# Optimization experiments

Hardware: AMD Instinct MI355X
Metric: run time of the kernel (lower is better)

## Reference

```python
import jax, jax.numpy as jnp
import numpy as np

N, F, B = 16384, 512, 4
H = 4          # attn heads
MR = 2         # mlp_ratio
GH = max(F // 4, 32)   # gate hidden = 128
SE = F // 8    # SE bottleneck
FH = 512       # fusion_hidden
E = 3          # num experts
EPS = 1e-5


def setup_inputs() -> dict:
    key = jax.random.key(0)
    ks = jax.random.split(key, 24)
    p = lambda k, s: 0.02 * jax.random.normal(k, s, dtype=jnp.float32)
    return {
        'branches': jax.random.normal(ks[0], (N, F, B), dtype=jnp.float32),
        'conv_pw_w': p(ks[1], (F, F)),          # Conv1d k=1, no bias
        'conv_dw_w': p(ks[2], (F, 3)),          # depthwise k=3
        'gn_w': jnp.ones((F,), jnp.float32), 'gn_b': jnp.zeros((F,), jnp.float32),
        'se_w1': p(ks[3], (SE, F)), 'se_w2': p(ks[4], (F, SE)),
        'ln_attn_w': jnp.ones((F,), jnp.float32), 'ln_attn_b': jnp.zeros((F,), jnp.float32),
        'in_proj_w': p(ks[5], (3 * F, F)), 'in_proj_b': jnp.zeros((3 * F,), jnp.float32),
        'attn_out_w': p(ks[6], (F, F)), 'attn_out_b': jnp.zeros((F,), jnp.float32),
        'ln_ffn_w': jnp.ones((F,), jnp.float32), 'ln_ffn_b': jnp.zeros((F,), jnp.float32),
        'ffn_w1': p(ks[7], (MR * F, F)), 'ffn_b1': jnp.zeros((MR * F,), jnp.float32),
        'ffn_w2': p(ks[8], (F, MR * F)), 'ffn_b2': jnp.zeros((F,), jnp.float32),
        'mlp_ln_w': jnp.ones((F,), jnp.float32), 'mlp_ln_b': jnp.zeros((F,), jnp.float32),
        'mlp_w1': p(ks[9], (MR * F, F)), 'mlp_b1': jnp.zeros((MR * F,), jnp.float32),
        'mlp_w2': p(ks[10], (F, MR * F)), 'mlp_b2': jnp.zeros((F,), jnp.float32),
        'gate_w1': p(ks[11], (GH, 2 * F)), 'gate_b1': jnp.zeros((GH,), jnp.float32),
        'gate_w2': p(ks[12], (E, GH)), 'gate_b2': jnp.zeros((E,), jnp.float32),
        'outp_w': p(ks[13], (FH, F)),
    }


def _ln(x, w, b):
    m = jnp.mean(x, -1, keepdims=True)
    v = jnp.mean((x - m) ** 2, -1, keepdims=True)
    return (x - m) * jax.lax.rsqrt(v + EPS) * w + b


def _gelu(x):
    return jax.nn.gelu(x, approximate=False)


def _forward(branches, conv_pw_w, conv_dw_w, gn_w, gn_b, se_w1, se_w2,
             ln_attn_w, ln_attn_b, in_proj_w, in_proj_b, attn_out_w, attn_out_b,
             ln_ffn_w, ln_ffn_b, ffn_w1, ffn_b1, ffn_w2, ffn_b2,
             mlp_ln_w, mlp_ln_b, mlp_w1, mlp_b1, mlp_w2, mlp_b2,
             gate_w1, gate_b1, gate_w2, gate_b2, outp_w):
    # ---- Conv expert ----
    x1 = jnp.einsum('fg,ngb->nfb', conv_pw_w, branches)          # pointwise conv
    xp = jnp.pad(x1, ((0, 0), (0, 0), (1, 1)))                    # depthwise k=3, pad=1
    w0, w1, w2 = (conv_dw_w[:, k][None, :, None] for k in range(3))
    x1 = w0 * xp[:, :, :-2] + w1 * xp[:, :, 1:-1] + w2 * xp[:, :, 2:]
    s = jnp.mean(x1, -1)                                          # SE squeeze (N,F)
    s = jax.nn.sigmoid(jax.nn.relu(s @ se_w1.T) @ se_w2.T)
    x1 = x1 * s[:, :, None]
    m = jnp.mean(x1, (1, 2), keepdims=True)                       # GroupNorm(1 group)
    v = jnp.mean((x1 - m) ** 2, (1, 2), keepdims=True)
    x1 = (x1 - m) * jax.lax.rsqrt(v + EPS) * gn_w[None, :, None] + gn_b[None, :, None]
    x1 = _gelu(x1)
    # ---- Attention expert (branches as tokens) ----
    t = jnp.swapaxes(branches, 1, 2)                              # (N,B,F)
    h = _ln(t, ln_attn_w, ln_attn_b)
    qkv = h @ in_proj_w.T + in_proj_b
    q, k, vv = jnp.split(qkv, 3, axis=-1)
    dh = F // H
    q = q.reshape(N, B, H, dh) * (dh ** -0.5)
    k = k.reshape(N, B, H, dh)
    vv = vv.reshape(N, B, H, dh)
    att = jax.nn.softmax(jnp.einsum('nqhd,nkhd->nhqk', q, k), axis=-1)
    ao = jnp.einsum('nhqk,nkhd->nqhd', att, vv).reshape(N, B, F)
    t = t + ao @ attn_out_w.T + attn_out_b
    h = _ln(t, ln_ffn_w, ln_ffn_b)
    t = t + _gelu(h @ ffn_w1.T + ffn_b1) @ ffn_w2.T + ffn_b2
    x2 = jnp.swapaxes(t, 1, 2)
    # ---- MLP expert ----
    t3 = jnp.swapaxes(branches, 1, 2)
    h3 = _ln(t3, mlp_ln_w, mlp_ln_b)
    t3 = t3 + _gelu(h3 @ mlp_w1.T + mlp_b1) @ mlp_w2.T + mlp_b2
    x3 = jnp.swapaxes(t3, 1, 2)
    # ---- Gating ----
    ctx = jnp.concatenate([jnp.mean(branches, -1), jnp.max(branches, -1)], axis=-1)
    logits = _gelu(ctx @ gate_w1.T + gate_b1) @ gate_w2.T + gate_b2
    alpha = jax.nn.softmax(logits, axis=-1)                       # (N,3)
    fused = (alpha[:, 0, None, None] * x1 + alpha[:, 1, None, None] * x2
             + alpha[:, 2, None, None] * x3)
    return jnp.einsum('of,nfb->nob', outp_w, fused)               # out_proj k=1 conv


def reference(branches, conv_pw_w, conv_dw_w, gn_w, gn_b, se_w1, se_w2,
              ln_attn_w, ln_attn_b, in_proj_w, in_proj_b, attn_out_w, attn_out_b,
              ln_ffn_w, ln_ffn_b, ffn_w1, ffn_b1, ffn_w2, ffn_b2,
              mlp_ln_w, mlp_ln_b, mlp_w1, mlp_b1, mlp_w2, mlp_b2,
              gate_w1, gate_b1, gate_w2, gate_b2, outp_w):
    return _forward(branches, conv_pw_w, conv_dw_w, gn_w, gn_b, se_w1, se_w2,
                    ln_attn_w, ln_attn_b, in_proj_w, in_proj_b, attn_out_w, attn_out_b,
                    ln_ffn_w, ln_ffn_b, ffn_w1, ffn_b1, ffn_w2, ffn_b2,
                    mlp_ln_w, mlp_ln_b, mlp_w1, mlp_b1, mlp_w2, mlp_b2,
                    gate_w1, gate_b1, gate_w2, gate_b2, outp_w)
```

## Files before the change

kernel.cpp:

```cpp
#include <hip/hip_runtime.h>
#include <math.h>


#define N_TOT 16384
#define EPSV 1e-5f

typedef unsigned short u16;
typedef unsigned int   u32;
typedef __attribute__((ext_vector_type(8))) short  short8;
typedef __attribute__((ext_vector_type(4))) float  floatx4;

__device__ __forceinline__ float gelu_exact(float x) {
    return 0.5f * x * (1.0f + erff(x * 0.70710678118654752440f));
}
__device__ __forceinline__ float wave_sum(float v) {
    #pragma unroll
    for (int o = 32; o > 0; o >>= 1) v += __shfl_xor(v, o);
    return v;
}
__device__ __forceinline__ u16 f2bf(float f) {
    u32 u = __float_as_uint(f);
    return (u16)((u + 0x7fffu + ((u >> 16) & 1u)) >> 16);
}
__device__ __forceinline__ u32 pack2(float lo, float hi) {
    return (u32)f2bf(lo) | ((u32)f2bf(hi) << 16);
}
__device__ __forceinline__ float bf1f(u16 u) { return __uint_as_float((u32)u << 16); }
__device__ __forceinline__ float2 bf2f2(u32 u) {
    return make_float2(__uint_as_float(u << 16), __uint_as_float(u & 0xffff0000u));
}
__device__ __forceinline__ void gload_lds16(const void* g, void* l) {
    __builtin_amdgcn_global_load_lds(
        (const __attribute__((address_space(1))) unsigned int*)g,
        (__attribute__((address_space(3))) unsigned int*)l, 16, 0, 0);
}

#define BARR() asm volatile("s_barrier" ::: "memory")
#define VMW(N) asm volatile("s_waitcnt vmcnt(" #N ")" ::: "memory")

#define W_CONVPW 0
#define W_INPROJ 262144
#define W_ATTNO  1048576
#define W_FFN1   1310720
#define W_FFN2   1835008
#define W_MLP1   2359296
#define W_MLP2   2883584
#define W_GATE1  3407872
#define W_SE1    3538944
#define W_SE2    3571712
#define W_OUTP   3604480
#define W_TOT    3866624

__global__ __launch_bounds__(256) void k_w2b(
        const float* __restrict__ p0, const float* __restrict__ p1,
        const float* __restrict__ p2, const float* __restrict__ p3,
        const float* __restrict__ p4, const float* __restrict__ p5,
        const float* __restrict__ p6, const float* __restrict__ p7,
        const float* __restrict__ p8, const float* __restrict__ p9,
        const float* __restrict__ p10, u16* __restrict__ dst)
{
    int i = blockIdx.x * 256 + threadIdx.x;
    if (i >= W_TOT) return;
    const float* s; int off;
    if      (i < W_INPROJ) { s = p0;  off = W_CONVPW; }
    else if (i < W_ATTNO)  { s = p1;  off = W_INPROJ; }
    else if (i < W_FFN1)   { s = p2;  off = W_ATTNO; }
    else if (i < W_FFN2)   { s = p3;  off = W_FFN1; }
    else if (i < W_MLP1)   { s = p4;  off = W_FFN2; }
    else if (i < W_MLP2)   { s = p5;  off = W_MLP1; }
    else if (i < W_GATE1)  { s = p6;  off = W_MLP2; }
    else if (i < W_SE1)    { s = p7;  off = W_GATE1; }
    else if (i < W_SE2)    { s = p8;  off = W_SE1; }
    else if (i < W_OUTP)   { s = p9;  off = W_SE2; }
    else                   { s = p10; off = W_OUTP; }
    dst[i] = f2bf(s[i - off]);
}

__global__ __launch_bounds__(256) void k_prep_ln(const float* __restrict__ br,
        int baseN, u16* __restrict__ Tb, u16* __restrict__ CTX,
        const float* __restrict__ law, const float* __restrict__ lab, u16* __restrict__ LNA,
        const float* __restrict__ lmw, const float* __restrict__ lmb, u16* __restrict__ LNM)
{
    __shared__ float lds[4][516];
    int t = threadIdx.x;
    const float* p = br + (size_t)(baseN + blockIdx.x) * 2048;
    u16* c = CTX + (size_t)blockIdx.x * 1024;
    #pragma unroll
    for (int i = 0; i < 2; ++i) {
        int f = t + i * 256;
        float4 v = *(const float4*)(p + f * 4);
        lds[0][f] = v.x; lds[1][f] = v.y; lds[2][f] = v.z; lds[3][f] = v.w;
        c[f]       = f2bf((v.x + v.y + v.z + v.w) * 0.25f);
        c[512 + f] = f2bf(fmaxf(fmaxf(v.x, v.y), fmaxf(v.z, v.w)));
    }
    __syncthreads();
    int b = t >> 6, lane = t & 63, f0 = lane * 8;
    float xv[8];
    #pragma unroll
    for (int i = 0; i < 8; ++i) xv[i] = lds[b][f0 + i];
    float s = 0.f;
    #pragma unroll
    for (int i = 0; i < 8; ++i) s += xv[i];
    s = wave_sum(s);
    float m = s * (1.f / 512.f);
    float q = 0.f;
    #pragma unroll
    for (int i = 0; i < 8; ++i) { float d = xv[i] - m; q += d * d; }
    q = wave_sum(q);
    float rs = rsqrtf(q * (1.f / 512.f) + EPSV);
    size_t row = (size_t)blockIdx.x * 4 + b;
    *(uint4*)(Tb + row * 512 + f0) = make_uint4(pack2(xv[0], xv[1]), pack2(xv[2], xv[3]),
                                                pack2(xv[4], xv[5]), pack2(xv[6], xv[7]));
    float o[8];
    #pragma unroll
    for (int i = 0; i < 8; ++i) o[i] = (xv[i] - m) * rs * law[f0 + i] + lab[f0 + i];
    *(uint4*)(LNA + row * 512 + f0) = make_uint4(pack2(o[0], o[1]), pack2(o[2], o[3]),
                                                 pack2(o[4], o[5]), pack2(o[6], o[7]));
    #pragma unroll
    for (int i = 0; i < 8; ++i) o[i] = (xv[i] - m) * rs * lmw[f0 + i] + lmb[f0 + i];
    *(uint4*)(LNM + row * 512 + f0) = make_uint4(pack2(o[0], o[1]), pack2(o[2], o[3]),
                                                 pack2(o[4], o[5]), pack2(o[6], o[7]));
}

__global__ __launch_bounds__(256) void k_ln_b(const u16* __restrict__ X,
        const float* __restrict__ w, const float* __restrict__ b, u16* __restrict__ O)
{
    int t = threadIdx.x;
    int wave = t >> 6, lane = t & 63;
    size_t r = (size_t)blockIdx.x * 4 + wave;
    int f0 = lane * 8;
    uint4 raw = *(const uint4*)(X + r * 512 + f0);
    float xv[8];
    { float2 a = bf2f2(raw.x); xv[0] = a.x; xv[1] = a.y; }
    { float2 a = bf2f2(raw.y); xv[2] = a.x; xv[3] = a.y; }
    { float2 a = bf2f2(raw.z); xv[4] = a.x; xv[5] = a.y; }
    { float2 a = bf2f2(raw.w); xv[6] = a.x; xv[7] = a.y; }
    float s = 0.f;
    #pragma unroll
    for (int i = 0; i < 8; ++i) s += xv[i];
    s = wave_sum(s);
    float m = s * (1.f / 512.f);
    float q = 0.f;
    #pragma unroll
    for (int i = 0; i < 8; ++i) { float d = xv[i] - m; q += d * d; }
    q = wave_sum(q);
    float rs = rsqrtf(q * (1.f / 512.f) + EPSV);
    float o[8];
    #pragma unroll
    for (int i = 0; i < 8; ++i) o[i] = (xv[i] - m) * rs * w[f0 + i] + b[f0 + i];
    *(uint4*)(O + r * 512 + f0) = make_uint4(pack2(o[0], o[1]), pack2(o[2], o[3]),
                                             pack2(o[4], o[5]), pack2(o[6], o[7]));
}


#define STAGE(SLOT, TILE) do {                                                \
    const u16* sm_ = ((SLOT) < 2) ? A : W;                                    \
    int rb_ = (((SLOT) < 2) ? m0 : n0) + ((SLOT) & 1) * 128;                  \
    int k0_ = (TILE) * 64;                                                    \
    u16* db_ = lds + (((TILE) & 1) * 32768) + (SLOT) * 8192;                  \
    _Pragma("unroll")                                                         \
    for (int l_ = 0; l_ < 2; ++l_) {                                          \
        int L_ = (l_ * 512 + tid) * 16;                                       \
        int row_ = L_ >> 7;                                                   \
        int ir_ = (L_ & 127) ^ ((row_ & 7) << 4);                             \
        gload_lds16(sm_ + (size_t)(rb_ + row_) * K + k0_ + (ir_ >> 1),        \
                    db_ + (L_ >> 1));                                         \
    } } while (0)

#define QUAD(MH, NH, STAGESTMT) do {                                          \
    const u16* lb_ = lds + cur * 32768;                                       \
    short8 a_[4][2], b_[2][2];                                                \
    _Pragma("unroll")                                                         \
    for (int mi = 0; mi < 4; ++mi)                                            \
        _Pragma("unroll")                                                     \
        for (int ks = 0; ks < 2; ++ks)                                        \
            a_[mi][ks] = *(const short8*)(lb_ + (MH) * 8192 + arow[mi] + gcol[ks]); \
    _Pragma("unroll")                                                         \
    for (int ni = 0; ni < 2; ++ni)                                            \
        _Pragma("unroll")                                                     \
        for (int ks = 0; ks < 2; ++ks)                                        \
            b_[ni][ks] = *(const short8*)(lb_ + 16384 + (NH) * 8192 + brow[ni] + gcol[ks]); \
    STAGESTMT;                                                                \
    BARR();                                                                   \
    __builtin_amdgcn_s_setprio(1);                                            \
    _Pragma("unroll")                                                         \
    for (int ks = 0; ks < 2; ++ks)                                            \
        _Pragma("unroll")                                                     \
        for (int mi = 0; mi < 4; ++mi)                                        \
            _Pragma("unroll")                                                 \
            for (int ni = 0; ni < 2; ++ni)                                    \
                acc[MH][NH][mi][ni] = __builtin_amdgcn_mfma_f32_16x16x32_bf16( \
                    a_[mi][ks], b_[ni][ks], acc[MH][NH][mi][ni], 0, 0, 0);    \
    __builtin_amdgcn_s_setprio(0);                                            \
} while (0)

template<int EPI, bool HAS_BIAS, bool HAS_RES, int STORE>
__global__ __launch_bounds__(512, 2) void k_gemm256(
        const u16* __restrict__ A, const u16* __restrict__ W,
        const float* __restrict__ bias, const u16* __restrict__ Res,
        void* __restrict__ Cout, int Ncols, int K, int baseN, int nTX)
{
    __shared__ __align__(16) u16 lds[65536];
    const int tid = threadIdx.x;
    const int wid = tid >> 6, lane = tid & 63;
    const int lr = lane & 15, kg = lane >> 4;
    const int wm = (wid >> 2) * 64;
    const int wn = (wid & 3) * 32;

    int nwg = gridDim.x, orig = blockIdx.x;
    int q = nwg >> 3, r = nwg & 7;
    int xcd = orig & 7, lin = orig >> 3;
    int wgid = (xcd < r ? xcd * (q + 1) : r * (q + 1) + (xcd - r) * q) + lin;
    const int m0 = (wgid / nTX) * 256, n0 = (wgid % nTX) * 256;

    int arow[4], brow[2], gcol[2];
    #pragma unroll
    for (int mi = 0; mi < 4; ++mi) arow[mi] = (wm + mi * 16 + lr) * 64;
    #pragma unroll
    for (int ni = 0; ni < 2; ++ni) brow[ni] = (wn + ni * 16 + lr) * 64;
    #pragma unroll
    for (int ks = 0; ks < 2; ++ks) gcol[ks] = (ks * 32 + kg * 8) ^ ((lr & 7) << 3);

    floatx4 acc[2][2][4][2] = {};

    STAGE(0, 0); STAGE(2, 0); STAGE(1, 0); STAGE(3, 0);

    const int NT = K >> 6;
    int cur = 0;
    for (int t = 0; t < NT - 1; ++t) {
        int nx = t + 1;
        VMW(4); BARR(); QUAD(0, 0, STAGE(0, nx));
        VMW(4); BARR(); QUAD(1, 0, STAGE(2, nx));
        VMW(4); BARR(); QUAD(0, 1, STAGE(1, nx));
                BARR(); QUAD(1, 1, STAGE(3, nx));
        cur ^= 1;
    }
    VMW(4); BARR(); QUAD(0, 0, (void)0);
    VMW(2); BARR(); QUAD(1, 0, (void)0);
    VMW(0); BARR(); QUAD(0, 1, (void)0);
            BARR(); QUAD(1, 1, (void)0);

    int rm = kg * 4;
    #pragma unroll
    for (int MH = 0; MH < 2; ++MH)
    #pragma unroll
    for (int NH = 0; NH < 2; ++NH)
    #pragma unroll
    for (int ni = 0; ni < 2; ++ni) {
        int n = n0 + NH * 128 + wn + ni * 16 + lr;
        float bv = HAS_BIAS ? bias[n] : 0.f;
        #pragma unroll
        for (int mi = 0; mi < 4; ++mi) {
            int mb = m0 + MH * 128 + wm + mi * 16 + rm;
            float vv[4];
            #pragma unroll
            for (int rr = 0; rr < 4; ++rr) {
                float v = acc[MH][NH][mi][ni][rr] + bv;
                if (EPI == 1) v = gelu_exact(v);
                else if (EPI == 2) v = fmaxf(v, 0.f);
                else if (EPI == 3) v = 1.f / (1.f + expf(-v));
                vv[rr] = v;
            }
            if (STORE == 2) {
                *(float4*)((float*)Cout + (size_t)(baseN + (mb >> 2)) * 2048 + (size_t)n * 4)
                    = make_float4(vv[0], vv[1], vv[2], vv[3]);
            } else {
                #pragma unroll
                for (int rr = 0; rr < 4; ++rr) {
                    float v = vv[rr];
                    if (HAS_RES) v += bf1f(Res[(size_t)(mb + rr) * Ncols + n]);
                    ((u16*)Cout)[(size_t)(mb + rr) * Ncols + n] = f2bf(v);
                }
            }
        }
    }
}

template<int EPI, bool HAS_BIAS, bool HAS_RES, int STORE>
__global__ __launch_bounds__(256) void k_mfma_gemm(
        const u16* __restrict__ A, const u16* __restrict__ W,
        const float* __restrict__ bias, const u16* __restrict__ Res,
        void* __restrict__ Cout, int M, int Ncols, int K, int baseN)
{
    __shared__ u16 As[128 * 32];
    __shared__ u16 Bs[128 * 32];
    int t = threadIdx.x;
    int wid = t >> 6, lane = t & 63;
    int wm = (wid >> 1) * 64, wn = (wid & 1) * 64;
    int m0 = blockIdx.y * 128, n0 = blockIdx.x * 128;
    int srow = t >> 2;
    int scol = (((t & 3) ^ ((srow >> 1) & 3)) * 8);
    int aR0 = min(m0 + srow, M - 1),      aR1 = min(m0 + 64 + srow, M - 1);
    int bR0 = min(n0 + srow, Ncols - 1),  bR1 = min(n0 + 64 + srow, Ncols - 1);
    const u16* Ap0 = A + (size_t)aR0 * K + scol;
    const u16* Ap1 = A + (size_t)aR1 * K + scol;
    const u16* Wp0 = W + (size_t)bR0 * K + scol;
    const u16* Wp1 = W + (size_t)bR1 * K + scol;
    u16* AsT0 = As + t * 8;  u16* AsT1 = As + 2048 + t * 8;
    u16* BsT0 = Bs + t * 8;  u16* BsT1 = Bs + 2048 + t * 8;

    int kg = lane >> 4, lr = lane & 15;
    int cb = kg ^ ((lr >> 1) & 3);
    const u16* aF = As + (wm + lr) * 32 + cb * 8;
    const u16* bF = Bs + (wn + lr) * 32 + cb * 8;

    floatx4 acc[4][4] = {};
    for (int k0 = 0; k0 < K; k0 += 32) {
        __syncthreads();
        gload_lds16(Ap0 + k0, AsT0);
        gload_lds16(Ap1 + k0, AsT1);
        gload_lds16(Wp0 + k0, BsT0);
        gload_lds16(Wp1 + k0, BsT1);
        __syncthreads();
        short8 a[4], b[4];
        #pragma unroll
        for (int i = 0; i < 4; ++i) {
            a[i] = *(const short8*)(aF + i * 512);
            b[i] = *(const short8*)(bF + i * 512);
        }
        #pragma unroll
        for (int i = 0; i < 4; ++i)
            #pragma unroll
            for (int j = 0; j < 4; ++j)
                acc[i][j] = __builtin_amdgcn_mfma_f32_16x16x32_bf16(a[i], b[j], acc[i][j], 0, 0, 0);
    }
    int rm = (lane >> 4) * 4;
    #pragma unroll
    for (int j = 0; j < 4; ++j) {
        int n = n0 + wn + j * 16 + lr;
        float bv = HAS_BIAS ? bias[min(n, Ncols - 1)] : 0.f;
        #pragma unroll
        for (int i = 0; i < 4; ++i) {
            int mb = m0 + wm + i * 16 + rm;
            float vv[4];
            #pragma unroll
            for (int r = 0; r < 4; ++r) {
                float v = acc[i][j][r] + bv;
                if (EPI == 1) v = gelu_exact(v);
                else if (EPI == 2) v = fmaxf(v, 0.f);
                else if (EPI == 3) v = 1.f / (1.f + expf(-v));
                vv[r] = v;
            }
            #pragma unroll
            for (int r = 0; r < 4; ++r) {
                int m = mb + r;
                if (m < M && n < Ncols) {
                    float v = vv[r];
                    if (HAS_RES) v += bf1f(Res[(size_t)m * Ncols + n]);
                    if (STORE == 0) ((float*)Cout)[(size_t)m * Ncols + n] = v;
                    else            ((u16*)Cout)[(size_t)m * Ncols + n] = f2bf(v);
                }
            }
        }
    }
}

__global__ __launch_bounds__(256) void k_attn(const u16* __restrict__ QKV,
        u16* __restrict__ AO)
{
    int t = threadIdx.x;
    int h = t >> 6, lane = t & 63;
    size_t n = (size_t)blockIdx.x;
    const u16* base = QKV + n * 4 * 1536 + h * 128 + lane * 2;
    float2 q[4], k[4], v[4];
    #pragma unroll
    for (int b = 0; b < 4; ++b) {
        q[b] = bf2f2(*(const u32*)(base + b * 1536));
        k[b] = bf2f2(*(const u32*)(base + b * 1536 + 512));
        v[b] = bf2f2(*(const u32*)(base + b * 1536 + 1024));
    }
    const float scale = 0.08838834764831845f;
    float sc[4][4];
    #pragma unroll
    for (int qb = 0; qb < 4; ++qb)
        #pragma unroll
        for (int kb = 0; kb < 4; ++kb) {
            float p = q[qb].x * k[kb].x + q[qb].y * k[kb].y;
            sc[qb][kb] = wave_sum(p) * scale;
        }
    #pragma unroll
    for (int qb = 0; qb < 4; ++qb) {
        float mx = fmaxf(fmaxf(sc[qb][0], sc[qb][1]), fmaxf(sc[qb][2], sc[qb][3]));
        float e0 = expf(sc[qb][0] - mx), e1 = expf(sc[qb][1] - mx);
        float e2 = expf(sc[qb][2] - mx), e3 = expf(sc[qb][3] - mx);
        float inv = 1.f / (e0 + e1 + e2 + e3);
        float ox = (e0 * v[0].x + e1 * v[1].x + e2 * v[2].x + e3 * v[3].x) * inv;
        float oy = (e0 * v[0].y + e1 * v[1].y + e2 * v[2].y + e3 * v[3].y) * inv;
        *(u32*)(AO + (n * 4 + qb) * 512 + h * 128 + lane * 2) = pack2(ox, oy);
    }
}

__global__ __launch_bounds__(256) void k_dw(u16* __restrict__ XP,
        const float* __restrict__ dw, u16* __restrict__ S)
{
    size_t ls = blockIdx.x;
    int t = threadIdx.x;
    u16* p = XP + ls * 2048;
    int f = t * 2;
    float2 x0 = bf2f2(*(const u32*)(p + f));
    float2 x1 = bf2f2(*(const u32*)(p + 512 + f));
    float2 x2 = bf2f2(*(const u32*)(p + 1024 + f));
    float2 x3 = bf2f2(*(const u32*)(p + 1536 + f));
    float2 w0 = make_float2(dw[f * 3 + 0], dw[f * 3 + 3]);
    float2 w1 = make_float2(dw[f * 3 + 1], dw[f * 3 + 4]);
    float2 w2 = make_float2(dw[f * 3 + 2], dw[f * 3 + 5]);
    float2 y0 = make_float2(w1.x * x0.x + w2.x * x1.x, w1.y * x0.y + w2.y * x1.y);
    float2 y1 = make_float2(w0.x * x0.x + w1.x * x1.x + w2.x * x2.x,
                            w0.y * x0.y + w1.y * x1.y + w2.y * x2.y);
    float2 y2 = make_float2(w0.x * x1.x + w1.x * x2.x + w2.x * x3.x,
                            w0.y * x1.y + w1.y * x2.y + w2.y * x3.y);
    float2 y3 = make_float2(w0.x * x2.x + w1.x * x3.x, w0.y * x2.y + w1.y * x3.y);
    *(u32*)(p + f)        = pack2(y0.x, y0.y);
    *(u32*)(p + 512 + f)  = pack2(y1.x, y1.y);
    *(u32*)(p + 1024 + f) = pack2(y2.x, y2.y);
    *(u32*)(p + 1536 + f) = pack2(y3.x, y3.y);
    *(u32*)(S + ls * 512 + f) = pack2((y0.x + y1.x + y2.x + y3.x) * 0.25f,
                                      (y0.y + y1.y + y2.y + y3.y) * 0.25f);
}

__global__ __launch_bounds__(256) void k_gnfin_fuse(
        const u16* __restrict__ XP, const u16* __restrict__ SIG,
        const float* __restrict__ gnw, const float* __restrict__ gnb,
        const u16* __restrict__ X2, const u16* __restrict__ X3,
        const float* __restrict__ alpha, int baseN, u16* __restrict__ FU)
{
    __shared__ float red[8];
    size_t ls = blockIdx.x;
    int t = threadIdx.x;
    int wave = t >> 6, lane = t & 63;
    int f = t * 2;
    const u16* p = XP + ls * 2048;
    float2 sg = bf2f2(*(const u32*)(SIG + ls * 512 + f));
    float2 xr[4];
    #pragma unroll
    for (int b = 0; b < 4; ++b) {
        float2 x = bf2f2(*(const u32*)(p + b * 512 + f));
        xr[b] = make_float2(x.x * sg.x, x.y * sg.y);
    }
    float s = 0.f;
    #pragma unroll
    for (int b = 0; b < 4; ++b) s += xr[b].x + xr[b].y;
    s = wave_sum(s);
    if (lane == 0) red[wave] = s;
    __syncthreads();
    float m = (red[0] + red[1] + red[2] + red[3]) * (1.f / 2048.f);
    float q = 0.f;
    #pragma unroll
    for (int b = 0; b < 4; ++b) {
        float dx = xr[b].x - m, dy = xr[b].y - m;
        q += dx * dx + dy * dy;
    }
    q = wave_sum(q);
    if (lane == 0) red[4 + wave] = q;
    __syncthreads();
    float rs = rsqrtf((red[4] + red[5] + red[6] + red[7]) * (1.f / 2048.f) + EPSV);
    const float* a = alpha + (size_t)(baseN + ls) * 3;
    float a0 = a[0], a1 = a[1], a2 = a[2];
    float gw0 = gnw[f], gw1 = gnw[f + 1], gb0 = gnb[f], gb1 = gnb[f + 1];
    #pragma unroll
    for (int b = 0; b < 4; ++b) {
        float x1a = gelu_exact((xr[b].x - m) * rs * gw0 + gb0);
        float x1b = gelu_exact((xr[b].y - m) * rs * gw1 + gb1);
        float2 v2 = bf2f2(*(const u32*)(X2 + (ls * 4 + b) * 512 + f));
        float2 v3 = bf2f2(*(const u32*)(X3 + (ls * 4 + b) * 512 + f));
        *(u32*)(FU + (ls * 4 + b) * 512 + f) =
            pack2(a0 * x1a + a1 * v2.x + a2 * v3.x,
                  a0 * x1b + a1 * v2.y + a2 * v3.y);
    }
}

__global__ __launch_bounds__(256) void k_gate2(const u16* __restrict__ G1,
        const float* __restrict__ w2, const float* __restrict__ b2,
        float* __restrict__ alpha, int CH)
{
    int s = blockIdx.x * 256 + threadIdx.x;
    if (s >= CH) return;
    float l0 = b2[0], l1 = b2[1], l2 = b2[2];
    const u16* g = G1 + (size_t)s * 128;
    for (int j = 0; j < 128; j += 2) {
        float2 gg = bf2f2(*(const u32*)(g + j));
        l0 += gg.x * w2[j]       + gg.y * w2[j + 1];
        l1 += gg.x * w2[128 + j] + gg.y * w2[129 + j];
        l2 += gg.x * w2[256 + j] + gg.y * w2[257 + j];
    }
    float mx = fmaxf(l0, fmaxf(l1, l2));
    float e0 = expf(l0 - mx), e1 = expf(l1 - mx), e2 = expf(l2 - mx);
    float inv = 1.f / (e0 + e1 + e2);
    float* a = alpha + (size_t)s * 3;
    a[0] = e0 * inv; a[1] = e1 * inv; a[2] = e2 * inv;
}

extern "C" void kernel_launch(void* const* d_in, const int* in_sizes, int n_in,
                              void* d_out, int out_size, void* d_ws, size_t ws_size,
                              hipStream_t stream)
{
    (void)in_sizes; (void)n_in; (void)out_size;
    const float* br         = (const float*)d_in[0];
    const float* conv_pw_w  = (const float*)d_in[1];
    const float* conv_dw_w  = (const float*)d_in[2];
    const float* gn_w       = (const float*)d_in[3];
    const float* gn_b       = (const float*)d_in[4];
    const float* se_w1      = (const float*)d_in[5];
    const float* se_w2      = (const float*)d_in[6];
    const float* ln_attn_w  = (const float*)d_in[7];
    const float* ln_attn_b  = (const float*)d_in[8];
    const float* in_proj_w  = (const float*)d_in[9];
    const float* in_proj_b  = (const float*)d_in[10];
    const float* attn_out_w = (const float*)d_in[11];
    const float* attn_out_b = (const float*)d_in[12];
    const float* ln_ffn_w   = (const float*)d_in[13];
    const float* ln_ffn_b   = (const float*)d_in[14];
    const float* ffn_w1     = (const float*)d_in[15];
    const float* ffn_b1     = (const float*)d_in[16];
    const float* ffn_w2     = (const float*)d_in[17];
    const float* ffn_b2     = (const float*)d_in[18];
    const float* mlp_ln_w   = (const float*)d_in[19];
    const float* mlp_ln_b   = (const float*)d_in[20];
    const float* mlp_w1     = (const float*)d_in[21];
    const float* mlp_b1     = (const float*)d_in[22];
    const float* mlp_w2     = (const float*)d_in[23];
    const float* mlp_b2     = (const float*)d_in[24];
    const float* gate_w1    = (const float*)d_in[25];
    const float* gate_b1    = (const float*)d_in[26];
    const float* gate_w2    = (const float*)d_in[27];
    const float* gate_b2    = (const float*)d_in[28];
    const float* outp_w     = (const float*)d_in[29];
    float* out = (float*)d_out;

    char* ws = (char*)d_ws;
    float* alpha = (float*)ws;
    u16* Wb = (u16*)(ws + 196608);
    const size_t CB = 196608 + (size_t)W_TOT * 2;
    int CH = N_TOT;
    while (CH > 64 && CB + (size_t)CH * 49536ULL > ws_size) CH >>= 1;

    char* p = ws + CB;
    u16* Tb  = (u16*)p; p += (size_t)CH * 4096;
    u16* CTX = (u16*)p; p += (size_t)CH * 2048;
    u16* LNA = (u16*)p; p += (size_t)CH * 4096;
    u16* LNM = (u16*)p; p += (size_t)CH * 4096;
    u16* QKV = (u16*)p; p += (size_t)CH * 12288;
    u16* AO  = (u16*)p; p += (size_t)CH * 4096;
    u16* T2b = (u16*)p; p += (size_t)CH * 4096;
    u16* X2b = (u16*)p; p += (size_t)CH * 4096;
    u16* X3b = (u16*)p; p += (size_t)CH * 4096;
    u16* XPb = (u16*)p; p += (size_t)CH * 4096;
    u16* S   = (u16*)p; p += (size_t)CH * 1024;
    u16* H1  = (u16*)p; p += (size_t)CH * 128;
    u16* SIGb= (u16*)p; p += (size_t)CH * 1024;
    u16* G1  = (u16*)p; p += (size_t)CH * 256;
    u16* U   = QKV;
    u16* LNF = LNA;
    u16* FU  = LNM;

    k_w2b<<<(W_TOT + 255) / 256, 256, 0, stream>>>(
        conv_pw_w, in_proj_w, attn_out_w, ffn_w1, ffn_w2, mlp_w1, mlp_w2,
        gate_w1, se_w1, se_w2, outp_w, Wb);

    const int Ri = CH * 4;
    auto g128 = [](int M, int Nc) { return dim3((Nc + 127) / 128, (M + 127) / 128); };
    auto g256 = [](int M, int Nc) { return dim3((M / 256) * (Nc / 256)); };

    for (int c0 = 0; c0 < N_TOT; c0 += CH) {
        k_prep_ln<<<CH, 256, 0, stream>>>(br, c0, Tb, CTX,
                                          ln_attn_w, ln_attn_b, LNA,
                                          mlp_ln_w, mlp_ln_b, LNM);
        k_mfma_gemm<1, true, false, 1><<<g128(CH, 128), 256, 0, stream>>>(
            CTX, Wb + W_GATE1, gate_b1, nullptr, G1, CH, 128, 1024, 0);
        k_gate2<<<(CH + 255) / 256, 256, 0, stream>>>(G1, gate_w2, gate_b2,
                                                      alpha + (size_t)c0 * 3, CH);
        k_gemm256<0, true, false, 1><<<g256(Ri, 1536), 512, 0, stream>>>(
            LNA, Wb + W_INPROJ, in_proj_b, nullptr, QKV, 1536, 512, 0, 6);
        k_attn<<<CH, 256, 0, stream>>>(QKV, AO);
        k_gemm256<0, true, true, 1><<<g256(Ri, 512), 512, 0, stream>>>(
            AO, Wb + W_ATTNO, attn_out_b, Tb, T2b, 512, 512, 0, 2);
        k_ln_b<<<Ri / 4, 256, 0, stream>>>(T2b, ln_ffn_w, ln_ffn_b, LNF);
        k_gemm256<1, true, false, 1><<<g256(Ri, 1024), 512, 0, stream>>>(
            LNF, Wb + W_FFN1, ffn_b1, nullptr, U, 1024, 512, 0, 4);
        k_gemm256<0, true, true, 1><<<g256(Ri, 512), 512, 0, stream>>>(
            U, Wb + W_FFN2, ffn_b2, T2b, X2b, 512, 1024, 0, 2);
        k_gemm256<1, true, false, 1><<<g256(Ri, 1024), 512, 0, stream>>>(
            LNM, Wb + W_MLP1, mlp_b1, nullptr, U, 1024, 512, 0, 4);
        k_gemm256<0, true, true, 1><<<g256(Ri, 512), 512, 0, stream>>>(
            U, Wb + W_MLP2, mlp_b2, Tb, X3b, 512, 1024, 0, 2);
        k_gemm256<0, false, false, 1><<<g256(Ri, 512), 512, 0, stream>>>(
            Tb, Wb + W_CONVPW, nullptr, nullptr, XPb, 512, 512, 0, 2);
        k_dw<<<CH, 256, 0, stream>>>(XPb, conv_dw_w, S);
        k_mfma_gemm<2, false, false, 1><<<g128(CH, 64), 256, 0, stream>>>(
            S, Wb + W_SE1, nullptr, nullptr, H1, CH, 64, 512, 0);
        k_mfma_gemm<3, false, false, 1><<<g128(CH, 512), 256, 0, stream>>>(
            H1, Wb + W_SE2, nullptr, nullptr, SIGb, CH, 512, 64, 0);
        k_gnfin_fuse<<<CH, 256, 0, stream>>>(XPb, SIGb, gn_w, gn_b,
                                             X2b, X3b, alpha, c0, FU);
        k_gemm256<0, false, false, 2><<<g256(Ri, 512), 512, 0, stream>>>(
            FU, Wb + W_OUTP, nullptr, nullptr, out, 512, 512, c0, 2);
    }
}
```

Measured before the change: 1.160 ms.

## Restructure 256x256 GEMM into two K-half phases and batch prep_ln samples

The 256x256 GEMM drops its four-quadrant schedule. Each wave now owns a full 128x64 output tile and computes over two K-halves of 32 per 64-wide tile, with a new swizzled LDS layout. This gives each wave more MFMAs per LDS fragment load and halves the barriers per K tile, at the cost of a larger accumulator and more register pressure. The prep/layernorm kernel now handles four samples per block, so it launches fewer, larger blocks with more LDS each.

```diff
diff --git a/kernel.cpp b/kernel.cpp
--- a/kernel.cpp
+++ b/kernel.cpp
@@ -81,45 +81,54 @@
         const float* __restrict__ law, const float* __restrict__ lab, u16* __restrict__ LNA,
         const float* __restrict__ lmw, const float* __restrict__ lmb, u16* __restrict__ LNM)
 {
-    __shared__ float lds[4][516];
+    __shared__ float lds[4][4][516];
     int t = threadIdx.x;
-    const float* p = br + (size_t)(baseN + blockIdx.x) * 2048;
-    u16* c = CTX + (size_t)blockIdx.x * 1024;
-    #pragma unroll
-    for (int i = 0; i < 2; ++i) {
-        int f = t + i * 256;
-        float4 v = *(const float4*)(p + f * 4);
-        lds[0][f] = v.x; lds[1][f] = v.y; lds[2][f] = v.z; lds[3][f] = v.w;
-        c[f]       = f2bf((v.x + v.y + v.z + v.w) * 0.25f);
-        c[512 + f] = f2bf(fmaxf(fmaxf(v.x, v.y), fmaxf(v.z, v.w)));
+    int s0 = blockIdx.x * 4;
+    #pragma unroll
+    for (int s = 0; s < 4; ++s) {
+        const float* p = br + (size_t)(baseN + s0 + s) * 2048;
+        u16* c = CTX + (size_t)(s0 + s) * 1024;
+        #pragma unroll
+        for (int i = 0; i < 2; ++i) {
+            int f = t + i * 256;
+            float4 v = *(const float4*)(p + f * 4);
+            lds[s][0][f] = v.x; lds[s][1][f] = v.y; lds[s][2][f] = v.z; lds[s][3][f] = v.w;
+            c[f]       = f2bf((v.x + v.y + v.z + v.w) * 0.25f);
+            c[512 + f] = f2bf(fmaxf(fmaxf(v.x, v.y), fmaxf(v.z, v.w)));
+        }
     }
     __syncthreads();
-    int b = t >> 6, lane = t & 63, f0 = lane * 8;
-    float xv[8];
-    #pragma unroll
-    for (int i = 0; i < 8; ++i) xv[i] = lds[b][f0 + i];
-    float s = 0.f;
-    #pragma unroll
-    for (int i = 0; i < 8; ++i) s += xv[i];
-    s = wave_sum(s);
-    float m = s * (1.f / 512.f);
-    float q = 0.f;
-    #pragma unroll
-    for (int i = 0; i < 8; ++i) { float d = xv[i] - m; q += d * d; }
-    q = wave_sum(q);
-    float rs = rsqrtf(q * (1.f / 512.f) + EPSV);
-    size_t row = (size_t)blockIdx.x * 4 + b;
-    *(uint4*)(Tb + row * 512 + f0) = make_uint4(pack2(xv[0], xv[1]), pack2(xv[2], xv[3]),
-                                                pack2(xv[4], xv[5]), pack2(xv[6], xv[7]));
-    float o[8];
-    #pragma unroll
-    for (int i = 0; i < 8; ++i) o[i] = (xv[i] - m) * rs * law[f0 + i] + lab[f0 + i];
-    *(uint4*)(LNA + row * 512 + f0) = make_uint4(pack2(o[0], o[1]), pack2(o[2], o[3]),
-                                                 pack2(o[4], o[5]), pack2(o[6], o[7]));
-    #pragma unroll
-    for (int i = 0; i < 8; ++i) o[i] = (xv[i] - m) * rs * lmw[f0 + i] + lmb[f0 + i];
-    *(uint4*)(LNM + row * 512 + f0) = make_uint4(pack2(o[0], o[1]), pack2(o[2], o[3]),
-                                                 pack2(o[4], o[5]), pack2(o[6], o[7]));
+    int wv = t >> 6, lane = t & 63, f0 = lane * 8;
+    #pragma unroll
+    for (int p4i = 0; p4i < 4; ++p4i) {
+        int idx = wv * 4 + p4i;
+        int s = idx >> 2, b = idx & 3;
+        float xv[8];
+        #pragma unroll
+        for (int i = 0; i < 8; ++i) xv[i] = lds[s][b][f0 + i];
+        float sm = 0.f;
+        #pragma unroll
+        for (int i = 0; i < 8; ++i) sm += xv[i];
+        sm = wave_sum(sm);
+        float m = sm * (1.f / 512.f);
+        float q = 0.f;
+        #pragma unroll
+        for (int i = 0; i < 8; ++i) { float d = xv[i] - m; q += d * d; }
+        q = wave_sum(q);
+        float rs = rsqrtf(q * (1.f / 512.f) + EPSV);
+        size_t row = (size_t)(s0 + s) * 4 + b;
+        *(uint4*)(Tb + row * 512 + f0) = make_uint4(pack2(xv[0], xv[1]), pack2(xv[2], xv[3]),
+                                                    pack2(xv[4], xv[5]), pack2(xv[6], xv[7]));
+        float o[8];
+        #pragma unroll
+        for (int i = 0; i < 8; ++i) o[i] = (xv[i] - m) * rs * law[f0 + i] + lab[f0 + i];
+        *(uint4*)(LNA + row * 512 + f0) = make_uint4(pack2(o[0], o[1]), pack2(o[2], o[3]),
+                                                     pack2(o[4], o[5]), pack2(o[6], o[7]));
+        #pragma unroll
+        for (int i = 0; i < 8; ++i) o[i] = (xv[i] - m) * rs * lmw[f0 + i] + lmb[f0 + i];
+        *(uint4*)(LNM + row * 512 + f0) = make_uint4(pack2(o[0], o[1]), pack2(o[2], o[3]),
+                                                     pack2(o[4], o[5]), pack2(o[6], o[7]));
+    }
 }
 
 __global__ __launch_bounds__(256) void k_ln_b(const u16* __restrict__ X,
@@ -153,44 +162,42 @@
 }
 
 
-#define STAGE(SLOT, TILE) do {                                                \
-    const u16* sm_ = ((SLOT) < 2) ? A : W;                                    \
-    int rb_ = (((SLOT) < 2) ? m0 : n0) + ((SLOT) & 1) * 128;                  \
-    int k0_ = (TILE) * 64;                                                    \
-    u16* db_ = lds + (((TILE) & 1) * 32768) + (SLOT) * 8192;                  \
+#define STAGE(S, TILE) do {                                                   \
+    const int bb_ = ((TILE) & 1) * 32768 + (S) * 16384;                       \
+    const int k0_ = (TILE) * 64 + (S) * 32;                                   \
     _Pragma("unroll")                                                         \
     for (int l_ = 0; l_ < 2; ++l_) {                                          \
-        int L_ = (l_ * 512 + tid) * 16;                                       \
-        int row_ = L_ >> 7;                                                   \
-        int ir_ = (L_ & 127) ^ ((row_ & 7) << 4);                             \
-        gload_lds16(sm_ + (size_t)(rb_ + row_) * K + k0_ + (ir_ >> 1),        \
-                    db_ + (L_ >> 1));                                         \
+        int E_ = (l_ * 512 + tid) * 8;                                        \
+        int r_ = E_ >> 6, c_ = E_ & 63;                                       \
+        int cp_ = c_ ^ ((r_ & 7) << 3);                                       \
+        gload_lds16(A + (size_t)(m0 + r_ + ((cp_ >> 5) << 7)) * K + k0_ + (cp_ & 31), \
+                    lds + bb_ + E_);                                          \
+    }                                                                         \
+    _Pragma("unroll")                                                         \
+    for (int l_ = 0; l_ < 2; ++l_) {                                          \
+        int E_ = (l_ * 512 + tid) * 8;                                        \
+        int r_ = E_ >> 6, c_ = E_ & 63;                                       \
+        int cp_ = c_ ^ ((r_ & 7) << 3);                                       \
+        gload_lds16(W + (size_t)(n0 + r_ + ((cp_ >> 5) << 7)) * K + k0_ + (cp_ & 31), \
+                    lds + bb_ + 8192 + E_);                                   \
     } } while (0)
 
-#define QUAD(MH, NH, STAGESTMT) do {                                          \
-    const u16* lb_ = lds + cur * 32768;                                       \
-    short8 a_[4][2], b_[2][2];                                                \
+#define PHASE(S, STAGESTMT) do {                                              \
+    const u16* lb_ = lds + cur * 32768 + (S) * 16384;                         \
+    short8 a_[8], b_[4];                                                      \
     _Pragma("unroll")                                                         \
-    for (int mi = 0; mi < 4; ++mi)                                            \
-        _Pragma("unroll")                                                     \
-        for (int ks = 0; ks < 2; ++ks)                                        \
-            a_[mi][ks] = *(const short8*)(lb_ + (MH) * 8192 + arow[mi] + gcol[ks]); \
+    for (int mi = 0; mi < 8; ++mi) a_[mi] = *(const short8*)(lb_ + aoff[mi]); \
     _Pragma("unroll")                                                         \
-    for (int ni = 0; ni < 2; ++ni)                                            \
-        _Pragma("unroll")                                                     \
-        for (int ks = 0; ks < 2; ++ks)                                        \
-            b_[ni][ks] = *(const short8*)(lb_ + 16384 + (NH) * 8192 + brow[ni] + gcol[ks]); \
+    for (int ni = 0; ni < 4; ++ni) b_[ni] = *(const short8*)(lb_ + 8192 + boff[ni]); \
     STAGESTMT;                                                                \
     BARR();                                                                   \
     __builtin_amdgcn_s_setprio(1);                                            \
     _Pragma("unroll")                                                         \
-    for (int ks = 0; ks < 2; ++ks)                                            \
+    for (int mi = 0; mi < 8; ++mi)                                            \
         _Pragma("unroll")                                                     \
-        for (int mi = 0; mi < 4; ++mi)                                        \
-            _Pragma("unroll")                                                 \
-            for (int ni = 0; ni < 2; ++ni)                                    \
-                acc[MH][NH][mi][ni] = __builtin_amdgcn_mfma_f32_16x16x32_bf16( \
-                    a_[mi][ks], b_[ni][ks], acc[MH][NH][mi][ni], 0, 0, 0);    \
+        for (int ni = 0; ni < 4; ++ni)                                        \
+            acc[mi][ni] = __builtin_amdgcn_mfma_f32_16x16x32_bf16(            \
+                a_[mi], b_[ni], acc[mi][ni], 0, 0, 0);                        \
     __builtin_amdgcn_s_setprio(0);                                            \
 } while (0)
 
@@ -204,8 +211,8 @@
     const int tid = threadIdx.x;
     const int wid = tid >> 6, lane = tid & 63;
     const int lr = lane & 15, kg = lane >> 4;
-    const int wm = (wid >> 2) * 64;
-    const int wn = (wid & 3) * 32;
+    const int wm = (wid >> 2) * 128;
+    const int wn = (wid & 3) * 64;
 
     int nwg = gridDim.x, orig = blockIdx.x;
     int q = nwg >> 3, r = nwg & 7;
@@ -213,49 +220,45 @@
     int wgid = (xcd < r ? xcd * (q + 1) : r * (q + 1) + (xcd - r) * q) + lin;
     const int m0 = (wgid / nTX) * 256, n0 = (wgid % nTX) * 256;
 
-    int arow[4], brow[2], gcol[2];
-    #pragma unroll
-    for (int mi = 0; mi < 4; ++mi) arow[mi] = (wm + mi * 16 + lr) * 64;
-    #pragma unroll
-    for (int ni = 0; ni < 2; ++ni) brow[ni] = (wn + ni * 16 + lr) * 64;
-    #pragma unroll
-    for (int ks = 0; ks < 2; ++ks) gcol[ks] = (ks * 32 + kg * 8) ^ ((lr & 7) << 3);
-
-    floatx4 acc[2][2][4][2] = {};
-
-    STAGE(0, 0); STAGE(2, 0); STAGE(1, 0); STAGE(3, 0);
+    int aoff[8], boff[4];
+    #pragma unroll
+    for (int mi = 0; mi < 8; ++mi) {
+        int R = wm + mi * 16 + lr;
+        int rr_ = R & 127;
+        aoff[mi] = rr_ * 64 + ((((R >> 7) << 5) + kg * 8) ^ ((rr_ & 7) << 3));
+    }
+    #pragma unroll
+    for (int ni = 0; ni < 4; ++ni) {
+        int R = wn + ni * 16 + lr;
+        int rr_ = R & 127;
+        boff[ni] = rr_ * 64 + ((((R >> 7) << 5) + kg * 8) ^ ((rr_ & 7) << 3));
+    }
+
+    floatx4 acc[8][4] = {};
+
+    STAGE(0, 0); STAGE(1, 0);
 
     const int NT = K >> 6;
     int cur = 0;
     for (int t = 0; t < NT - 1; ++t) {
-        int nx = t + 1;
-        VMW(4); BARR(); QUAD(0, 0, STAGE(0, nx));
-        VMW(4); BARR(); QUAD(1, 0, STAGE(2, nx));
-        VMW(4); BARR(); QUAD(0, 1, STAGE(1, nx));
-                BARR(); QUAD(1, 1, STAGE(3, nx));
+        VMW(4); BARR(); PHASE(0, STAGE(0, t + 1));
+        VMW(4); BARR(); PHASE(1, STAGE(1, t + 1));
         cur ^= 1;
     }
-    VMW(4); BARR(); QUAD(0, 0, (void)0);
-    VMW(2); BARR(); QUAD(1, 0, (void)0);
-    VMW(0); BARR(); QUAD(0, 1, (void)0);
-            BARR(); QUAD(1, 1, (void)0);
-
-    int rm = kg * 4;
-    #pragma unroll
-    for (int MH = 0; MH < 2; ++MH)
-    #pragma unroll
-    for (int NH = 0; NH < 2; ++NH)
-    #pragma unroll
-    for (int ni = 0; ni < 2; ++ni) {
-        int n = n0 + NH * 128 + wn + ni * 16 + lr;
+    VMW(4); BARR(); PHASE(0, (void)0);
+    VMW(0); BARR(); PHASE(1, (void)0);
+
+    #pragma unroll
+    for (int ni = 0; ni < 4; ++ni) {
+        int n = n0 + wn + ni * 16 + lr;
         float bv = HAS_BIAS ? bias[n] : 0.f;
         #pragma unroll
-        for (int mi = 0; mi < 4; ++mi) {
-            int mb = m0 + MH * 128 + wm + mi * 16 + rm;
+        for (int mi = 0; mi < 8; ++mi) {
+            int mb = m0 + wm + mi * 16 + kg * 4;
             float vv[4];
             #pragma unroll
             for (int rr = 0; rr < 4; ++rr) {
-                float v = acc[MH][NH][mi][ni][rr] + bv;
+                float v = acc[mi][ni][rr] + bv;
                 if (EPI == 1) v = gelu_exact(v);
                 else if (EPI == 2) v = fmaxf(v, 0.f);
                 else if (EPI == 3) v = 1.f / (1.f + expf(-v));
@@ -562,9 +565,9 @@
     auto g256 = [](int M, int Nc) { return dim3((M / 256) * (Nc / 256)); };
 
     for (int c0 = 0; c0 < N_TOT; c0 += CH) {
-        k_prep_ln<<<CH, 256, 0, stream>>>(br, c0, Tb, CTX,
-                                          ln_attn_w, ln_attn_b, LNA,
-                                          mlp_ln_w, mlp_ln_b, LNM);
+        k_prep_ln<<<CH / 4, 256, 0, stream>>>(br, c0, Tb, CTX,
+                                              ln_attn_w, ln_attn_b, LNA,
+                                              mlp_ln_w, mlp_ln_b, LNM);
         k_mfma_gemm<1, true, false, 1><<<g128(CH, 128), 256, 0, stream>>>(
             CTX, Wb + W_GATE1, gate_b1, nullptr, G1, CH, 128, 1024, 0);
         k_gate2<<<(CH + 255) / 256, 256, 0, stream>>>(G1, gate_w2, gate_b2,
```

Result: slower. 1.508 ms (+30.0%).

## Fuse depthwise conv into pointwise GEMM epilogue and alias buffers into output

Applied to the files above, without the earlier changes.

Removes the standalone depthwise-conv kernel by applying the k=3 depthwise filter and the per-sample mean inside the conv_pw GEMM epilogue. This avoids a full read-modify-write pass over the XP buffer. Intermediates X2/T2/X3 are placed in the unused output buffer and several scratch buffers share memory, shrinking per-chunk workspace so larger chunks fit. The prep/LN kernel now handles four samples per block. The trade-offs are scattered 2-byte stores in the epilogue and a risk that, when the work is split into several chunks, later chunks' intermediates overwrite outputs already written.

```diff
diff --git a/kernel.cpp b/kernel.cpp
--- a/kernel.cpp
+++ b/kernel.cpp
@@ -81,45 +81,54 @@
         const float* __restrict__ law, const float* __restrict__ lab, u16* __restrict__ LNA,
         const float* __restrict__ lmw, const float* __restrict__ lmb, u16* __restrict__ LNM)
 {
-    __shared__ float lds[4][516];
+    __shared__ float lds[4][4][516];
     int t = threadIdx.x;
-    const float* p = br + (size_t)(baseN + blockIdx.x) * 2048;
-    u16* c = CTX + (size_t)blockIdx.x * 1024;
-    #pragma unroll
-    for (int i = 0; i < 2; ++i) {
-        int f = t + i * 256;
-        float4 v = *(const float4*)(p + f * 4);
-        lds[0][f] = v.x; lds[1][f] = v.y; lds[2][f] = v.z; lds[3][f] = v.w;
-        c[f]       = f2bf((v.x + v.y + v.z + v.w) * 0.25f);
-        c[512 + f] = f2bf(fmaxf(fmaxf(v.x, v.y), fmaxf(v.z, v.w)));
+    int s0 = blockIdx.x * 4;
+    #pragma unroll
+    for (int s = 0; s < 4; ++s) {
+        const float* p = br + (size_t)(baseN + s0 + s) * 2048;
+        u16* c = CTX + (size_t)(s0 + s) * 1024;
+        #pragma unroll
+        for (int i = 0; i < 2; ++i) {
+            int f = t + i * 256;
+            float4 v = *(const float4*)(p + f * 4);
+            lds[s][0][f] = v.x; lds[s][1][f] = v.y; lds[s][2][f] = v.z; lds[s][3][f] = v.w;
+            c[f]       = f2bf((v.x + v.y + v.z + v.w) * 0.25f);
+            c[512 + f] = f2bf(fmaxf(fmaxf(v.x, v.y), fmaxf(v.z, v.w)));
+        }
     }
     __syncthreads();
-    int b = t >> 6, lane = t & 63, f0 = lane * 8;
-    float xv[8];
-    #pragma unroll
-    for (int i = 0; i < 8; ++i) xv[i] = lds[b][f0 + i];
-    float s = 0.f;
-    #pragma unroll
-    for (int i = 0; i < 8; ++i) s += xv[i];
-    s = wave_sum(s);
-    float m = s * (1.f / 512.f);
-    float q = 0.f;
-    #pragma unroll
-    for (int i = 0; i < 8; ++i) { float d = xv[i] - m; q += d * d; }
-    q = wave_sum(q);
-    float rs = rsqrtf(q * (1.f / 512.f) + EPSV);
-    size_t row = (size_t)blockIdx.x * 4 + b;
-    *(uint4*)(Tb + row * 512 + f0) = make_uint4(pack2(xv[0], xv[1]), pack2(xv[2], xv[3]),
-                                                pack2(xv[4], xv[5]), pack2(xv[6], xv[7]));
-    float o[8];
-    #pragma unroll
-    for (int i = 0; i < 8; ++i) o[i] = (xv[i] - m) * rs * law[f0 + i] + lab[f0 + i];
-    *(uint4*)(LNA + row * 512 + f0) = make_uint4(pack2(o[0], o[1]), pack2(o[2], o[3]),
-                                                 pack2(o[4], o[5]), pack2(o[6], o[7]));
-    #pragma unroll
-    for (int i = 0; i < 8; ++i) o[i] = (xv[i] - m) * rs * lmw[f0 + i] + lmb[f0 + i];
-    *(uint4*)(LNM + row * 512 + f0) = make_uint4(pack2(o[0], o[1]), pack2(o[2], o[3]),
-                                                 pack2(o[4], o[5]), pack2(o[6], o[7]));
+    int wv = t >> 6, lane = t & 63, f0 = lane * 8;
+    #pragma unroll
+    for (int p4i = 0; p4i < 4; ++p4i) {
+        int idx = wv * 4 + p4i;
+        int s = idx >> 2, b = idx & 3;
+        float xv[8];
+        #pragma unroll
+        for (int i = 0; i < 8; ++i) xv[i] = lds[s][b][f0 + i];
+        float sm = 0.f;
+        #pragma unroll
+        for (int i = 0; i < 8; ++i) sm += xv[i];
+        sm = wave_sum(sm);
+        float m = sm * (1.f / 512.f);
+        float q = 0.f;
+        #pragma unroll
+        for (int i = 0; i < 8; ++i) { float d = xv[i] - m; q += d * d; }
+        q = wave_sum(q);
+        float rs = rsqrtf(q * (1.f / 512.f) + EPSV);
+        size_t row = (size_t)(s0 + s) * 4 + b;
+        *(uint4*)(Tb + row * 512 + f0) = make_uint4(pack2(xv[0], xv[1]), pack2(xv[2], xv[3]),
+                                                    pack2(xv[4], xv[5]), pack2(xv[6], xv[7]));
+        float o[8];
+        #pragma unroll
+        for (int i = 0; i < 8; ++i) o[i] = (xv[i] - m) * rs * law[f0 + i] + lab[f0 + i];
+        *(uint4*)(LNA + row * 512 + f0) = make_uint4(pack2(o[0], o[1]), pack2(o[2], o[3]),
+                                                     pack2(o[4], o[5]), pack2(o[6], o[7]));
+        #pragma unroll
+        for (int i = 0; i < 8; ++i) o[i] = (xv[i] - m) * rs * lmw[f0 + i] + lmb[f0 + i];
+        *(uint4*)(LNM + row * 512 + f0) = make_uint4(pack2(o[0], o[1]), pack2(o[2], o[3]),
+                                                     pack2(o[4], o[5]), pack2(o[6], o[7]));
+    }
 }
 
 __global__ __launch_bounds__(256) void k_ln_b(const u16* __restrict__ X,
@@ -198,7 +207,8 @@
 __global__ __launch_bounds__(512, 2) void k_gemm256(
         const u16* __restrict__ A, const u16* __restrict__ W,
         const float* __restrict__ bias, const u16* __restrict__ Res,
-        void* __restrict__ Cout, int Ncols, int K, int baseN, int nTX)
+        void* __restrict__ Cout, int Ncols, int K, int baseN, int nTX,
+        const float* __restrict__ dwp, u16* __restrict__ Sout)
 {
     __shared__ __align__(16) u16 lds[65536];
     const int tid = threadIdx.x;
@@ -249,6 +259,8 @@
     for (int ni = 0; ni < 2; ++ni) {
         int n = n0 + NH * 128 + wn + ni * 16 + lr;
         float bv = HAS_BIAS ? bias[n] : 0.f;
+        float w0, w1, w2;
+        if (STORE == 3) { w0 = dwp[n * 3]; w1 = dwp[n * 3 + 1]; w2 = dwp[n * 3 + 2]; }
         #pragma unroll
         for (int mi = 0; mi < 4; ++mi) {
             int mb = m0 + MH * 128 + wm + mi * 16 + rm;
@@ -264,6 +276,17 @@
             if (STORE == 2) {
                 *(float4*)((float*)Cout + (size_t)(baseN + (mb >> 2)) * 2048 + (size_t)n * 4)
                     = make_float4(vv[0], vv[1], vv[2], vv[3]);
+            } else if (STORE == 3) {
+                float y0 = w1 * vv[0] + w2 * vv[1];
+                float y1 = w0 * vv[0] + w1 * vv[1] + w2 * vv[2];
+                float y2 = w0 * vv[1] + w1 * vv[2] + w2 * vv[3];
+                float y3 = w0 * vv[2] + w1 * vv[3];
+                u16* xp = (u16*)Cout + (size_t)mb * Ncols + n;
+                xp[0] = f2bf(y0);
+                xp[Ncols] = f2bf(y1);
+                xp[2 * Ncols] = f2bf(y2);
+                xp[3 * Ncols] = f2bf(y3);
+                Sout[(size_t)(mb >> 2) * Ncols + n] = f2bf((y0 + y1 + y2 + y3) * 0.25f);
             } else {
                 #pragma unroll
                 for (int rr = 0; rr < 4; ++rr) {
@@ -388,34 +411,6 @@
         float oy = (e0 * v[0].y + e1 * v[1].y + e2 * v[2].y + e3 * v[3].y) * inv;
         *(u32*)(AO + (n * 4 + qb) * 512 + h * 128 + lane * 2) = pack2(ox, oy);
     }
-}
-
-__global__ __launch_bounds__(256) void k_dw(u16* __restrict__ XP,
-        const float* __restrict__ dw, u16* __restrict__ S)
-{
-    size_t ls = blockIdx.x;
-    int t = threadIdx.x;
-    u16* p = XP + ls * 2048;
-    int f = t * 2;
-    float2 x0 = bf2f2(*(const u32*)(p + f));
-    float2 x1 = bf2f2(*(const u32*)(p + 512 + f));
-    float2 x2 = bf2f2(*(const u32*)(p + 1024 + f));
-    float2 x3 = bf2f2(*(const u32*)(p + 1536 + f));
-    float2 w0 = make_float2(dw[f * 3 + 0], dw[f * 3 + 3]);
-    float2 w1 = make_float2(dw[f * 3 + 1], dw[f * 3 + 4]);
-    float2 w2 = make_float2(dw[f * 3 + 2], dw[f * 3 + 5]);
-    float2 y0 = make_float2(w1.x * x0.x + w2.x * x1.x, w1.y * x0.y + w2.y * x1.y);
-    float2 y1 = make_float2(w0.x * x0.x + w1.x * x1.x + w2.x * x2.x,
-                            w0.y * x0.y + w1.y * x1.y + w2.y * x2.y);
-    float2 y2 = make_float2(w0.x * x1.x + w1.x * x2.x + w2.x * x3.x,
-                            w0.y * x1.y + w1.y * x2.y + w2.y * x3.y);
-    float2 y3 = make_float2(w0.x * x2.x + w1.x * x3.x, w0.y * x2.y + w1.y * x3.y);
-    *(u32*)(p + f)        = pack2(y0.x, y0.y);
-    *(u32*)(p + 512 + f)  = pack2(y1.x, y1.y);
-    *(u32*)(p + 1024 + f) = pack2(y2.x, y2.y);
-    *(u32*)(p + 1536 + f) = pack2(y3.x, y3.y);
-    *(u32*)(S + ls * 512 + f) = pack2((y0.x + y1.x + y2.x + y3.x) * 0.25f,
-                                      (y0.y + y1.y + y2.y + y3.y) * 0.25f);
 }
 
 __global__ __launch_bounds__(256) void k_gnfin_fuse(
@@ -532,26 +527,25 @@
     u16* Wb = (u16*)(ws + 196608);
     const size_t CB = 196608 + (size_t)W_TOT * 2;
     int CH = N_TOT;
-    while (CH > 64 && CB + (size_t)CH * 49536ULL > ws_size) CH >>= 1;
+    while (CH > 64 && CB + (size_t)CH * 31104ULL > ws_size) CH >>= 1;
 
     char* p = ws + CB;
-    u16* Tb  = (u16*)p; p += (size_t)CH * 4096;
-    u16* CTX = (u16*)p; p += (size_t)CH * 2048;
-    u16* LNA = (u16*)p; p += (size_t)CH * 4096;
-    u16* LNM = (u16*)p; p += (size_t)CH * 4096;
-    u16* QKV = (u16*)p; p += (size_t)CH * 12288;
-    u16* AO  = (u16*)p; p += (size_t)CH * 4096;
-    u16* T2b = (u16*)p; p += (size_t)CH * 4096;
-    u16* X2b = (u16*)p; p += (size_t)CH * 4096;
-    u16* X3b = (u16*)p; p += (size_t)CH * 4096;
-    u16* XPb = (u16*)p; p += (size_t)CH * 4096;
-    u16* S   = (u16*)p; p += (size_t)CH * 1024;
-    u16* H1  = (u16*)p; p += (size_t)CH * 128;
-    u16* SIGb= (u16*)p; p += (size_t)CH * 1024;
-    u16* G1  = (u16*)p; p += (size_t)CH * 256;
-    u16* U   = QKV;
-    u16* LNF = LNA;
-    u16* FU  = LNM;
+    u16* Tb   = (u16*)p; p += (size_t)CH * 4096;
+    char* CTXS = p;      p += (size_t)CH * 2048;
+    u16* LNA  = (u16*)p; p += (size_t)CH * 4096;
+    u16* LNM  = (u16*)p; p += (size_t)CH * 4096;
+    u16* QKV  = (u16*)p; p += (size_t)CH * 12288;
+    u16* AOXP = (u16*)p; p += (size_t)CH * 4096;
+    u16* H1   = (u16*)p; p += (size_t)CH * 128;
+    u16* G1   = (u16*)p; p += (size_t)CH * 256;
+    u16* CTX  = (u16*)CTXS;
+    u16* S    = (u16*)CTXS;
+    u16* SIGb = (u16*)(CTXS + (size_t)CH * 1024);
+    u16* U    = QKV;
+    u16* LNF  = LNA;
+    u16* FU   = LNM;
+
+    u16* O16 = (u16*)d_out;
 
     k_w2b<<<(W_TOT + 255) / 256, 256, 0, stream>>>(
         conv_pw_w, in_proj_w, attn_out_w, ffn_w1, ffn_w2, mlp_w1, mlp_w2,
@@ -562,37 +556,39 @@
     auto g256 = [](int M, int Nc) { return dim3((M / 256) * (Nc / 256)); };
 
     for (int c0 = 0; c0 < N_TOT; c0 += CH) {
-        k_prep_ln<<<CH, 256, 0, stream>>>(br, c0, Tb, CTX,
-                                          ln_attn_w, ln_attn_b, LNA,
-                                          mlp_ln_w, mlp_ln_b, LNM);
+        u16* X2b  = O16 + (size_t)c0 * 2048;
+        u16* T2X3 = O16 + (size_t)N_TOT * 2048 + (size_t)c0 * 2048;
+
+        k_prep_ln<<<CH / 4, 256, 0, stream>>>(br, c0, Tb, CTX,
+                                              ln_attn_w, ln_attn_b, LNA,
+                                              mlp_ln_w, mlp_ln_b, LNM);
         k_mfma_gemm<1, true, false, 1><<<g128(CH, 128), 256, 0, stream>>>(
             CTX, Wb + W_GATE1, gate_b1, nullptr, G1, CH, 128, 1024, 0);
         k_gate2<<<(CH + 255) / 256, 256, 0, stream>>>(G1, gate_w2, gate_b2,
                                                       alpha + (size_t)c0 * 3, CH);
         k_gemm256<0, true, false, 1><<<g256(Ri, 1536), 512, 0, stream>>>(
-            LNA, Wb + W_INPROJ, in_proj_b, nullptr, QKV, 1536, 512, 0, 6);
-        k_attn<<<CH, 256, 0, stream>>>(QKV, AO);
+            LNA, Wb + W_INPROJ, in_proj_b, nullptr, QKV, 1536, 512, 0, 6, nullptr, nullptr);
+        k_attn<<<CH, 256, 0, stream>>>(QKV, AOXP);
         k_gemm256<0, true, true, 1><<<g256(Ri, 512), 512, 0, stream>>>(
-            AO, Wb + W_ATTNO, attn_out_b, Tb, T2b, 512, 512, 0, 2);
-        k_ln_b<<<Ri / 4, 256, 0, stream>>>(T2b, ln_ffn_w, ln_ffn_b, LNF);
+            AOXP, Wb + W_ATTNO, attn_out_b, Tb, T2X3, 512, 512, 0, 2, nullptr, nullptr);
+        k_ln_b<<<Ri / 4, 256, 0, stream>>>(T2X3, ln_ffn_w, ln_ffn_b, LNF);
         k_gemm256<1, true, false, 1><<<g256(Ri, 1024), 512, 0, stream>>>(
-            LNF, Wb + W_FFN1, ffn_b1, nullptr, U, 1024, 512, 0, 4);
+            LNF, Wb + W_FFN1, ffn_b1, nullptr, U, 1024, 512, 0, 4, nullptr, nullptr);
         k_gemm256<0, true, true, 1><<<g256(Ri, 512), 512, 0, stream>>>(
-            U, Wb + W_FFN2, ffn_b2, T2b, X2b, 512, 1024, 0, 2);
+            U, Wb + W_FFN2, ffn_b2, T2X3, X2b, 512, 1024, 0, 2, nullptr, nullptr);
         k_gemm256<1, true, false, 1><<<g256(Ri, 1024), 512, 0, stream>>>(
-            LNM, Wb + W_MLP1, mlp_b1, nullptr, U, 1024, 512, 0, 4);
+            LNM, Wb + W_MLP1, mlp_b1, nullptr, U, 1024, 512, 0, 4, nullptr, nullptr);
         k_gemm256<0, true, true, 1><<<g256(Ri, 512), 512, 0, stream>>>(
-            U, Wb + W_MLP2, mlp_b2, Tb, X3b, 512, 1024, 0, 2);
-        k_gemm256<0, false, false, 1><<<g256(Ri, 512), 512, 0, stream>>>(
-            Tb, Wb + W_CONVPW, nullptr, nullptr, XPb, 512, 512, 0, 2);
-        k_dw<<<CH, 256, 0, stream>>>(XPb, conv_dw_w, S);
+            U, Wb + W_MLP2, mlp_b2, Tb, T2X3, 512, 1024, 0, 2, nullptr, nullptr);
+        k_gemm256<0, false, false, 3><<<g256(Ri, 512), 512, 0, stream>>>(
+            Tb, Wb + W_CONVPW, nullptr, nullptr, AOXP, 512, 512, 0, 2, conv_dw_w, S);
         k_mfma_gemm<2, false, false, 1><<<g128(CH, 64), 256, 0, stream>>>(
             S, Wb + W_SE1, nullptr, nullptr, H1, CH, 64, 512, 0);
         k_mfma_gemm<3, false, false, 1><<<g128(CH, 512), 256, 0, stream>>>(
             H1, Wb + W_SE2, nullptr, nullptr, SIGb, CH, 512, 64, 0);
-        k_gnfin_fuse<<<CH, 256, 0, stream>>>(XPb, SIGb, gn_w, gn_b,
-                                             X2b, X3b, alpha, c0, FU);
+        k_gnfin_fuse<<<CH, 256, 0, stream>>>(AOXP, SIGb, gn_w, gn_b,
+                                             X2b, T2X3, alpha, c0, FU);
         k_gemm256<0, false, false, 2><<<g256(Ri, 512), 512, 0, stream>>>(
-            FU, Wb + W_OUTP, nullptr, nullptr, out, 512, 512, c0, 2);
-    }
-}
+            FU, Wb + W_OUTP, nullptr, nullptr, out, 512, 512, c0, 2, nullptr, nullptr);
+    }
+}
```

Result: faster. 1.036 ms (-10.6%).
